# Kernel optimization log

Measured on AMD Instinct MI355X. Metric: run time of the kernel, lower is better.

The kernel has to match this reference:

```python
import jax, jax.numpy as jnp
import numpy as np

N = 50000
E = 800000
IN_F = 128
OUT_F = 128


def setup_inputs() -> dict:
    key = jax.random.key(0)
    k1, k2, k3, k4, k5 = jax.random.split(key, 5)
    x = jax.random.normal(k1, (N, IN_F), dtype=jnp.float32)
    # sparse adjacency as COO edge list: row = dst (aggregating node), col = src
    edge_index = jax.random.randint(k2, (2, E), 0, N, dtype=jnp.int64)
    edge_weight = jax.random.uniform(k3, (E,), dtype=jnp.float32)
    # nn.Linear(in_features, out_features): W is [out, in], b is [out]
    W = jax.random.normal(k4, (OUT_F, IN_F), dtype=jnp.float32) * (1.0 / np.sqrt(IN_F))
    b = jax.random.normal(k5, (OUT_F,), dtype=jnp.float32) * 0.01
    return {"x": x, "edge_index": edge_index, "edge_weight": edge_weight, "W": W, "b": b}


def reference(x, edge_index, edge_weight, W, b):
    # hidden = self.linear(x)  -> [N, out]
    hidden = jnp.einsum("ni,oi->no", x, W) + b
    # out = adj @ hidden (SpMM): out[dst] += w_e * hidden[src]
    dst = edge_index[0]
    src = edge_index[1]
    msgs = edge_weight[:, None] * hidden[src]  # [E, out]
    out = jax.ops.segment_sum(msgs, dst, num_segments=x.shape[0])
    return out
```

## Files before the change

kernel.cpp:

```cpp
#include <hip/hip_runtime.h>
#include <hip/hip_bf16.h>

#define N_NODES 50000
#define N_EDGES 800000
#define FEAT    128
#define N_TILES (N_NODES / 16)
#define GEMM_BLOCKS 784
#define MAXD    32
#define OVF_CAP 16384
#define NODES_PER_GRP 6250
#define CHUNK   2048
#define NCHUNK  ((N_EDGES + CHUNK - 1) / CHUNK)

using short8  = __attribute__((ext_vector_type(8))) short;
using float4v = __attribute__((ext_vector_type(4))) float;


__device__ __forceinline__ unsigned short f2b(float f) {
    __hip_bfloat16 h = __float2bfloat16(f);
    return __builtin_bit_cast(unsigned short, h);
}

__global__ void k_init(const int* __restrict__ ei, int* __restrict__ flag,
                       int* __restrict__ fill) {
    int i = blockIdx.x * blockDim.x + threadIdx.x;
    if (i < N_NODES) fill[i] = 0;
    if (blockIdx.x == 0 && threadIdx.x < 64) {
        unsigned long long m = __ballot(ei[2 * threadIdx.x + 1] != 0);
        if (threadIdx.x == 0) { flag[0] = (m == 0ULL) ? 1 : 0; flag[1] = 0; }
    }
}

__global__ __launch_bounds__(256) void k_fused(const float* __restrict__ x,
                                               const float* __restrict__ W,
                                               const float* __restrict__ bias,
                                               unsigned short* __restrict__ hidden,
                                               const int* __restrict__ ei,
                                               const float* __restrict__ wt,
                                               int* __restrict__ flag,
                                               int* __restrict__ fill,
                                               unsigned int* __restrict__ slots,
                                               int2* __restrict__ ovf) {
    __shared__ __align__(16) unsigned short Wlds[128 * 136];
    const int t = threadIdx.x;

    if (blockIdx.x < GEMM_BLOCKS) {
        for (int j = 0; j < 16; ++j) {
            int idx4 = j * 256 + t;
            float4v wv = *(const float4v*)(W + (size_t)idx4 * 4);
            int r = (idx4 * 4) >> 7;
            int c = (idx4 * 4) & 127;
            unsigned short* p = &Wlds[r * 136 + c];
            p[0] = f2b(wv[0]); p[1] = f2b(wv[1]); p[2] = f2b(wv[2]); p[3] = f2b(wv[3]);
        }
        __syncthreads();

        const int wave = t >> 6;
        const int lane = t & 63;
        int tile = blockIdx.x * 4 + wave;
        if (tile >= N_TILES) tile = N_TILES - 1;
        const int rowBase = tile * 16;
        const int m    = lane & 15;
        const int quad = lane >> 4;

        float4v acc[8];
        for (int i = 0; i < 8; ++i) acc[i] = (float4v){0.f, 0.f, 0.f, 0.f};

        for (int kk = 0; kk < 4; ++kk) {
            const int k0 = kk * 32 + quad * 8;
            const float* ap = x + (size_t)(rowBase + m) * FEAT + k0;
            float4v a0 = *(const float4v*)(ap);
            float4v a1 = *(const float4v*)(ap + 4);
            short8 af;
            for (int j = 0; j < 4; ++j) { af[j] = (short)f2b(a0[j]); af[4 + j] = (short)f2b(a1[j]); }
            for (int nt = 0; nt < 8; ++nt) {
                short8 bf = *(const short8*)&Wlds[(nt * 16 + m) * 136 + k0];
                acc[nt] = __builtin_amdgcn_mfma_f32_16x16x32_bf16(af, bf, acc[nt], 0, 0, 0);
            }
        }

        const int r0 = rowBase + quad * 4;
        for (int nt = 0; nt < 8; ++nt) {
            const int col = nt * 16 + m;
            const float bc = bias[col];
            for (int r = 0; r < 4; ++r) {
                hidden[(size_t)(r0 + r) * FEAT + col] = f2b(acc[nt][r] + bc);
            }
        }
    } else {
        const int bid = blockIdx.x - GEMM_BLOCKS;
        const int grp = bid & 7;
        const int lo  = grp * NODES_PER_GRP;
        const int hi  = lo + NODES_PER_GRP;
        const int sh  = flag[0];
        const int e0  = (bid >> 3) * CHUNK + t;

        int dsts[8];
        #pragma unroll
        for (int i = 0; i < 8; ++i) {
            int e = e0 + i * 256;
            dsts[i] = (e < N_EDGES) ? ei[(size_t)e << sh] : -1;
        }
        #pragma unroll
        for (int i = 0; i < 8; ++i) {
            int e = e0 + i * 256;
            if (e >= N_EDGES) continue;
            int dst = dsts[i];
            if ((unsigned)dst >= N_NODES) dst = 0;
            if (dst < lo || dst >= hi) continue;
            int src = ei[(size_t)(N_EDGES + e) << sh];
            if ((unsigned)src >= N_NODES) src = 0;
            unsigned int rec = ((unsigned int)f2b(wt[e]) << 16) | (unsigned int)src;
            int pos = atomicAdd(&fill[dst], 1);
            if (pos < MAXD) {
                slots[(size_t)dst * MAXD + pos] = rec;
            } else {
                int op = atomicAdd(&flag[1], 1);
                if (op < OVF_CAP) { int2 r; r.x = dst; r.y = (int)rec; ovf[op] = r; }
            }
        }
    }
}

__global__ __launch_bounds__(256) void k_agg(const int* __restrict__ fill,
                                             const unsigned int* __restrict__ slots,
                                             const unsigned int* __restrict__ hid,
                                             const int* __restrict__ flag,
                                             const int2* __restrict__ ovf,
                                             float* __restrict__ out) {
    const int wave = threadIdx.x >> 6;
    const int lane = threadIdx.x & 63;
    const int node = blockIdx.x * 4 + wave;
    const int grp  = lane >> 4;
    const int sub  = lane & 15;

    const int degf = fill[node];
    const int deg  = (degf > MAXD) ? MAXD : degf;
    const unsigned int* sl = slots + (size_t)node * MAXD;

    float acc[8];
    #pragma unroll
    for (int j = 0; j < 8; ++j) acc[j] = 0.f;

    for (int e = 0; e < deg; e += 4) {
        uint4 recs = *(const uint4*)(sl + e);
        unsigned rec = (grp < 2) ? (grp == 0 ? recs.x : recs.y)
                                 : (grp == 2 ? recs.z : recs.w);
        const bool v = (e + grp) < deg;
        const float w = v ? __uint_as_float(rec & 0xffff0000u) : 0.f;
        const unsigned src = v ? (rec & 0xffffu) : 0u;
        uint4 h = *((const uint4*)(hid + (size_t)src * 64) + sub);
        acc[0] = fmaf(w, __uint_as_float((h.x & 0xffffu) << 16), acc[0]);
        acc[1] = fmaf(w, __uint_as_float(h.x & 0xffff0000u),     acc[1]);
        acc[2] = fmaf(w, __uint_as_float((h.y & 0xffffu) << 16), acc[2]);
        acc[3] = fmaf(w, __uint_as_float(h.y & 0xffff0000u),     acc[3]);
        acc[4] = fmaf(w, __uint_as_float((h.z & 0xffffu) << 16), acc[4]);
        acc[5] = fmaf(w, __uint_as_float(h.z & 0xffff0000u),     acc[5]);
        acc[6] = fmaf(w, __uint_as_float((h.w & 0xffffu) << 16), acc[6]);
        acc[7] = fmaf(w, __uint_as_float(h.w & 0xffff0000u),     acc[7]);
    }

    if (degf > MAXD) {
        int n = flag[1]; if (n > OVF_CAP) n = OVF_CAP;
        for (int i = 0; i < n; ++i) {
            int2 r = ovf[i];
            if (r.x != node || (i & 3) != grp) continue;
            unsigned rec = (unsigned)r.y;
            float w = __uint_as_float(rec & 0xffff0000u);
            unsigned src = rec & 0xffffu;
            uint4 h = *((const uint4*)(hid + (size_t)src * 64) + sub);
            acc[0] = fmaf(w, __uint_as_float((h.x & 0xffffu) << 16), acc[0]);
            acc[1] = fmaf(w, __uint_as_float(h.x & 0xffff0000u),     acc[1]);
            acc[2] = fmaf(w, __uint_as_float((h.y & 0xffffu) << 16), acc[2]);
            acc[3] = fmaf(w, __uint_as_float(h.y & 0xffff0000u),     acc[3]);
            acc[4] = fmaf(w, __uint_as_float((h.z & 0xffffu) << 16), acc[4]);
            acc[5] = fmaf(w, __uint_as_float(h.z & 0xffff0000u),     acc[5]);
            acc[6] = fmaf(w, __uint_as_float((h.w & 0xffffu) << 16), acc[6]);
            acc[7] = fmaf(w, __uint_as_float(h.w & 0xffff0000u),     acc[7]);
        }
    }

    #pragma unroll
    for (int j = 0; j < 8; ++j) {
        float a = acc[j];
        a += __shfl_xor(a, 16, 64);
        a += __shfl_xor(a, 32, 64);
        acc[j] = a;
    }

    if (lane < 16) {
        float* o = out + (size_t)node * FEAT + sub * 8;
        *(float4*)(o)     = make_float4(acc[0], acc[1], acc[2], acc[3]);
        *(float4*)(o + 4) = make_float4(acc[4], acc[5], acc[6], acc[7]);
    }
}

extern "C" void kernel_launch(void* const* d_in, const int* in_sizes, int n_in,
                              void* d_out, int out_size, void* d_ws, size_t ws_size,
                              hipStream_t stream) {
    const float* x  = (const float*)d_in[0];
    const int*   ei = (const int*)d_in[1];
    const float* ew = (const float*)d_in[2];
    const float* W  = (const float*)d_in[3];
    const float* b  = (const float*)d_in[4];
    float* out = (float*)d_out;

    int*  flag = (int*)d_ws;
    int*  fill = flag + 16;
    int2* ovf  = (int2*)(fill + 50048);
    unsigned int* slots = (unsigned int*)(ovf + OVF_CAP);
    unsigned short* hidden = (unsigned short*)(slots + (size_t)N_NODES * MAXD);

    k_init <<<(N_NODES + 255) / 256, 256, 0, stream>>>(ei, flag, fill);
    k_fused<<<GEMM_BLOCKS + NCHUNK * 8, 256, 0, stream>>>(x, W, b, hidden, ei, ew,
                                                          flag, fill, slots, ovf);
    k_agg  <<<N_NODES / 4, 256, 0, stream>>>(fill, slots, (const unsigned int*)hidden,
                                             flag, ovf, out);
}
```

Baseline: 173.3 us.

## Split fused gemm/scatter kernel and batch gather loads in aggregation

Splits the combined GEMM+edge-bucketing kernel into two separate launches (k_gemm and k_scatter), so the scatter no longer carries the 34KB LDS allocation of the GEMM branch and can run at higher occupancy. The scatter loads each dst inside its loop rather than preloading all eight. The aggregation kernel now decodes all 8 slot records up front, then issues the 8 hidden-row gathers in a fully unrolled loop. This aims for more memory-level parallelism, at the cost of always doing 8 iterations regardless of degree. It also loses the concurrency of GEMM and scatter within one launch and adds one extra launch.

```diff
diff --git a/kernel.cpp b/kernel.cpp
--- a/kernel.cpp
+++ b/kernel.cpp
@@ -5,7 +5,6 @@
 #define N_EDGES 800000
 #define FEAT    128
 #define N_TILES (N_NODES / 16)
-#define GEMM_BLOCKS 784
 #define MAXD    32
 #define OVF_CAP 16384
 #define NODES_PER_GRP 6250
@@ -31,93 +30,84 @@
     }
 }
 
-__global__ __launch_bounds__(256) void k_fused(const float* __restrict__ x,
-                                               const float* __restrict__ W,
-                                               const float* __restrict__ bias,
-                                               unsigned short* __restrict__ hidden,
-                                               const int* __restrict__ ei,
-                                               const float* __restrict__ wt,
-                                               int* __restrict__ flag,
-                                               int* __restrict__ fill,
-                                               unsigned int* __restrict__ slots,
-                                               int2* __restrict__ ovf) {
+__global__ __launch_bounds__(256) void k_gemm(const float* __restrict__ x,
+                                              const float* __restrict__ W,
+                                              const float* __restrict__ bias,
+                                              unsigned short* __restrict__ hidden) {
     __shared__ __align__(16) unsigned short Wlds[128 * 136];
     const int t = threadIdx.x;
-
-    if (blockIdx.x < GEMM_BLOCKS) {
-        for (int j = 0; j < 16; ++j) {
-            int idx4 = j * 256 + t;
-            float4v wv = *(const float4v*)(W + (size_t)idx4 * 4);
-            int r = (idx4 * 4) >> 7;
-            int c = (idx4 * 4) & 127;
-            unsigned short* p = &Wlds[r * 136 + c];
-            p[0] = f2b(wv[0]); p[1] = f2b(wv[1]); p[2] = f2b(wv[2]); p[3] = f2b(wv[3]);
-        }
-        __syncthreads();
-
-        const int wave = t >> 6;
-        const int lane = t & 63;
-        int tile = blockIdx.x * 4 + wave;
-        if (tile >= N_TILES) tile = N_TILES - 1;
-        const int rowBase = tile * 16;
-        const int m    = lane & 15;
-        const int quad = lane >> 4;
-
-        float4v acc[8];
-        for (int i = 0; i < 8; ++i) acc[i] = (float4v){0.f, 0.f, 0.f, 0.f};
-
-        for (int kk = 0; kk < 4; ++kk) {
-            const int k0 = kk * 32 + quad * 8;
-            const float* ap = x + (size_t)(rowBase + m) * FEAT + k0;
-            float4v a0 = *(const float4v*)(ap);
-            float4v a1 = *(const float4v*)(ap + 4);
-            short8 af;
-            for (int j = 0; j < 4; ++j) { af[j] = (short)f2b(a0[j]); af[4 + j] = (short)f2b(a1[j]); }
-            for (int nt = 0; nt < 8; ++nt) {
-                short8 bf = *(const short8*)&Wlds[(nt * 16 + m) * 136 + k0];
-                acc[nt] = __builtin_amdgcn_mfma_f32_16x16x32_bf16(af, bf, acc[nt], 0, 0, 0);
-            }
-        }
-
-        const int r0 = rowBase + quad * 4;
+    for (int j = 0; j < 16; ++j) {
+        int idx4 = j * 256 + t;
+        float4v wv = *(const float4v*)(W + (size_t)idx4 * 4);
+        int r = (idx4 * 4) >> 7;
+        int c = (idx4 * 4) & 127;
+        unsigned short* p = &Wlds[r * 136 + c];
+        p[0] = f2b(wv[0]); p[1] = f2b(wv[1]); p[2] = f2b(wv[2]); p[3] = f2b(wv[3]);
+    }
+    __syncthreads();
+
+    const int wave = t >> 6;
+    const int lane = t & 63;
+    int tile = blockIdx.x * 4 + wave;
+    if (tile >= N_TILES) tile = N_TILES - 1;
+    const int rowBase = tile * 16;
+    const int m    = lane & 15;
+    const int quad = lane >> 4;
+
+    float4v acc[8];
+    for (int i = 0; i < 8; ++i) acc[i] = (float4v){0.f, 0.f, 0.f, 0.f};
+
+    for (int kk = 0; kk < 4; ++kk) {
+        const int k0 = kk * 32 + quad * 8;
+        const float* ap = x + (size_t)(rowBase + m) * FEAT + k0;
+        float4v a0 = *(const float4v*)(ap);
+        float4v a1 = *(const float4v*)(ap + 4);
+        short8 af;
+        for (int j = 0; j < 4; ++j) { af[j] = (short)f2b(a0[j]); af[4 + j] = (short)f2b(a1[j]); }
         for (int nt = 0; nt < 8; ++nt) {
-            const int col = nt * 16 + m;
-            const float bc = bias[col];
-            for (int r = 0; r < 4; ++r) {
-                hidden[(size_t)(r0 + r) * FEAT + col] = f2b(acc[nt][r] + bc);
-            }
-        }
-    } else {
-        const int bid = blockIdx.x - GEMM_BLOCKS;
-        const int grp = bid & 7;
-        const int lo  = grp * NODES_PER_GRP;
-        const int hi  = lo + NODES_PER_GRP;
-        const int sh  = flag[0];
-        const int e0  = (bid >> 3) * CHUNK + t;
-
-        int dsts[8];
-        #pragma unroll
-        for (int i = 0; i < 8; ++i) {
-            int e = e0 + i * 256;
-            dsts[i] = (e < N_EDGES) ? ei[(size_t)e << sh] : -1;
-        }
-        #pragma unroll
-        for (int i = 0; i < 8; ++i) {
-            int e = e0 + i * 256;
-            if (e >= N_EDGES) continue;
-            int dst = dsts[i];
-            if ((unsigned)dst >= N_NODES) dst = 0;
-            if (dst < lo || dst >= hi) continue;
-            int src = ei[(size_t)(N_EDGES + e) << sh];
-            if ((unsigned)src >= N_NODES) src = 0;
-            unsigned int rec = ((unsigned int)f2b(wt[e]) << 16) | (unsigned int)src;
-            int pos = atomicAdd(&fill[dst], 1);
-            if (pos < MAXD) {
-                slots[(size_t)dst * MAXD + pos] = rec;
-            } else {
-                int op = atomicAdd(&flag[1], 1);
-                if (op < OVF_CAP) { int2 r; r.x = dst; r.y = (int)rec; ovf[op] = r; }
-            }
+            short8 bf = *(const short8*)&Wlds[(nt * 16 + m) * 136 + k0];
+            acc[nt] = __builtin_amdgcn_mfma_f32_16x16x32_bf16(af, bf, acc[nt], 0, 0, 0);
+        }
+    }
+
+    const int r0 = rowBase + quad * 4;
+    for (int nt = 0; nt < 8; ++nt) {
+        const int col = nt * 16 + m;
+        const float bc = bias[col];
+        for (int r = 0; r < 4; ++r) {
+            hidden[(size_t)(r0 + r) * FEAT + col] = f2b(acc[nt][r] + bc);
+        }
+    }
+}
+
+__global__ __launch_bounds__(256) void k_scatter(const int* __restrict__ ei,
+                                                 const float* __restrict__ wt,
+                                                 const int* __restrict__ flag,
+                                                 int* __restrict__ fill,
+                                                 unsigned int* __restrict__ slots,
+                                                 int2* __restrict__ ovf) {
+    const int grp = blockIdx.x & 7;
+    const int lo  = grp * NODES_PER_GRP;
+    const int hi  = lo + NODES_PER_GRP;
+    const int sh  = flag[0];
+    const int e0  = (blockIdx.x >> 3) * CHUNK + threadIdx.x;
+
+    #pragma unroll
+    for (int i = 0; i < CHUNK / 256; ++i) {
+        int e = e0 + i * 256;
+        if (e >= N_EDGES) break;
+        int dst = ei[(size_t)e << sh];
+        if ((unsigned)dst >= N_NODES) dst = 0;
+        if (dst < lo || dst >= hi) continue;
+        int src = ei[(size_t)(N_EDGES + e) << sh];
+        if ((unsigned)src >= N_NODES) src = 0;
+        unsigned int rec = ((unsigned int)f2b(wt[e]) << 16) | (unsigned int)src;
+        int pos = atomicAdd(&fill[dst], 1);
+        if (pos < MAXD) {
+            slots[(size_t)dst * MAXD + pos] = rec;
+        } else {
+            int op = atomicAdd((int*)&((int*)flag)[1], 1);
+            if (op < OVF_CAP) { int2 r; r.x = dst; r.y = (int)rec; ovf[op] = r; }
         }
     }
 }
@@ -142,14 +132,23 @@
     #pragma unroll
     for (int j = 0; j < 8; ++j) acc[j] = 0.f;
 
-    for (int e = 0; e < deg; e += 4) {
+    float    ws[8];
+    unsigned srcs[8];
+    #pragma unroll
+    for (int it = 0; it < 8; ++it) {
+        const int e = it * 4;
         uint4 recs = *(const uint4*)(sl + e);
         unsigned rec = (grp < 2) ? (grp == 0 ? recs.x : recs.y)
                                  : (grp == 2 ? recs.z : recs.w);
         const bool v = (e + grp) < deg;
-        const float w = v ? __uint_as_float(rec & 0xffff0000u) : 0.f;
-        const unsigned src = v ? (rec & 0xffffu) : 0u;
-        uint4 h = *((const uint4*)(hid + (size_t)src * 64) + sub);
+        ws[it]   = v ? __uint_as_float(rec & 0xffff0000u) : 0.f;
+        srcs[it] = v ? (rec & 0xffffu) : 0u;
+    }
+
+    #pragma unroll
+    for (int it = 0; it < 8; ++it) {
+        uint4 h = *((const uint4*)(hid + (size_t)srcs[it] * 64) + sub);
+        const float w = ws[it];
         acc[0] = fmaf(w, __uint_as_float((h.x & 0xffffu) << 16), acc[0]);
         acc[1] = fmaf(w, __uint_as_float(h.x & 0xffff0000u),     acc[1]);
         acc[2] = fmaf(w, __uint_as_float((h.y & 0xffffu) << 16), acc[2]);
@@ -211,9 +210,9 @@
     unsigned int* slots = (unsigned int*)(ovf + OVF_CAP);
     unsigned short* hidden = (unsigned short*)(slots + (size_t)N_NODES * MAXD);
 
-    k_init <<<(N_NODES + 255) / 256, 256, 0, stream>>>(ei, flag, fill);
-    k_fused<<<GEMM_BLOCKS + NCHUNK * 8, 256, 0, stream>>>(x, W, b, hidden, ei, ew,
-                                                          flag, fill, slots, ovf);
-    k_agg  <<<N_NODES / 4, 256, 0, stream>>>(fill, slots, (const unsigned int*)hidden,
-                                             flag, ovf, out);
-}
+    k_init   <<<(N_NODES + 255) / 256, 256, 0, stream>>>(ei, flag, fill);
+    k_gemm   <<<(N_TILES + 3) / 4, 256, 0, stream>>>(x, W, b, hidden);
+    k_scatter<<<NCHUNK * 8, 256, 0, stream>>>(ei, ew, flag, fill, slots, ovf);
+    k_agg    <<<N_NODES / 4, 256, 0, stream>>>(fill, slots, (const unsigned int*)hidden,
+                                               flag, ovf, out);
+}
```

Result: slower. 187.0 us (+7.9%).
